# Kernel tuning notes

Measured on AMD Instinct MI355X. Metric: run time of the kernel, lower is better.

The kernel has to match this reference:

```python
import jax, jax.numpy as jnp
import numpy as np

B, S, D = 32, 2048, 1024
E, K = 64, 8
N_TAGS = 128


def setup_inputs() -> dict:
    key = jax.random.key(0)
    k1, k2, k3, k4, k5, k6 = jax.random.split(key, 6)
    hidden_states = jax.random.normal(k1, (B, S, D), dtype=jnp.float32)
    subw_indices = jax.random.randint(k2, (B, E, K), 0, S, dtype=jnp.int32)
    subw_counts = jax.random.randint(k3, (B, E), 1, K + 1, dtype=jnp.int32)
    num_entities = jax.random.randint(k4, (B,), 1, E + 1, dtype=jnp.int32)
    fc_w = jax.random.normal(k5, (N_TAGS, D), dtype=jnp.float32) * (1.0 / np.sqrt(D))
    fc_b = jax.random.normal(k6, (N_TAGS,), dtype=jnp.float32) * 0.01
    return {
        "hidden_states": hidden_states,
        "subw_indices": subw_indices,
        "subw_counts": subw_counts,
        "num_entities": num_entities,
        "fc_w": fc_w,
        "fc_b": fc_b,
    }


def reference(hidden_states, subw_indices, subw_counts, num_entities, fc_w, fc_b):
    # Gather subword embeddings: [B, E, K, D]
    flat_idx = subw_indices.reshape(B, E * K)                      # [B, E*K]
    gathered = jnp.take_along_axis(
        hidden_states, flat_idx[:, :, None], axis=1
    ).reshape(B, E, K, D)
    # Mask padded subword slots and mean-pool per entity
    subw_mask = (jnp.arange(K)[None, None, :] < subw_counts[:, :, None])  # [B,E,K]
    subw_mask = subw_mask.astype(hidden_states.dtype)
    ent_emb = jnp.einsum("bekd,bek->bed", gathered, subw_mask)
    ent_emb = ent_emb / subw_counts[:, :, None].astype(hidden_states.dtype)
    # Zero-pad entities past num_entities (original pads with zero_emb)
    ent_mask = (jnp.arange(E)[None, :] < num_entities[:, None])    # [B,E]
    ent_emb = ent_emb * ent_mask[:, :, None].astype(hidden_states.dtype)
    # fc applied to all positions (padded rows yield the bias, as in original)
    logits = jnp.einsum("bed,td->bet", ent_emb, fc_w) + fc_b
    return logits
```

## Files before the change

### kernel.cpp

```cpp
#include <hip/hip_runtime.h>

#define BB 32
#define SS 2048
#define DD 1024
#define EE 64
#define KK 8
#define TT 128
#define MM (BB * EE)

#define KSPLIT 8
#define KCHUNK (DD / KSPLIT)
#define MT 32
#define LSTR 136

typedef __attribute__((ext_vector_type(8))) short short8;
typedef __attribute__((ext_vector_type(4))) float f32x4;

__device__ __forceinline__ unsigned short f2bf(float f) {
    union { float f; unsigned int u; } v; v.f = f;
    unsigned int u = v.u + 0x7FFFu + ((v.u >> 16) & 1u);
    return (unsigned short)(u >> 16);
}

__global__ __launch_bounds__(256) void bias_init_kernel(
    const float* __restrict__ fc_b,
    float* __restrict__ out)
{
    const int i = blockIdx.x * 256 + threadIdx.x;
    float4 b = *(const float4*)(fc_b + (i & 31) * 4);
    *(float4*)(out + 4 * (size_t)i) = b;
}

__global__ __launch_bounds__(256) void fc_fused_kernel(
    const float* __restrict__ hs,
    const int*   __restrict__ subw_idx,
    const int*   __restrict__ subw_cnt,
    const int*   __restrict__ num_ent,
    const float* __restrict__ fc_w,
    float* __restrict__ out)
{
    __shared__ unsigned short As[MT][LSTR];
    __shared__ unsigned short Bs[TT][LSTR];

    const int bx = blockIdx.x;
    const int mt = bx >> 3;
    const int ks = bx & (KSPLIT - 1);
    const int t  = threadIdx.x;
    const int wid  = t >> 6;
    const int lane = t & 63;
    const int k0 = ks * KCHUNK;

    {
        const int r   = t >> 3;
        const int sub = t & 7;
        const int be  = mt * MT + r;
        const int b   = be >> 6;
        const int e   = be & 63;
        const int cnt = subw_cnt[be];
        const int ne  = num_ent[b];
        const float scale = (e < ne) ? (1.0f / (float)cnt) : 0.0f;

        const int4* ip = (const int4*)(subw_idx + (size_t)be * KK);
        const int4 i0 = ip[0];
        const int4 i1 = ip[1];
        int idx[8] = { i0.x, i0.y, i0.z, i0.w, i1.x, i1.y, i1.z, i1.w };

        const float* base = hs + (size_t)b * SS * DD + k0 + sub * 16;

        float acc[16];
        #pragma unroll
        for (int j = 0; j < 16; ++j) acc[j] = 0.f;

        #pragma unroll
        for (int half = 0; half < 2; ++half) {
            float4 v[4][4];
            #pragma unroll
            for (int k = 0; k < 4; ++k) {
                const int kk = half * 4 + k;
                const int s = (kk < cnt) ? idx[kk] : idx[0];
                const float4* p = (const float4*)(base + (size_t)s * DD);
                v[k][0] = p[0]; v[k][1] = p[1]; v[k][2] = p[2]; v[k][3] = p[3];
            }
            #pragma unroll
            for (int k = 0; k < 4; ++k) {
                const float w = ((half * 4 + k) < cnt) ? 1.0f : 0.0f;
                #pragma unroll
                for (int j = 0; j < 4; ++j) {
                    acc[4*j+0] = fmaf(w, v[k][j].x, acc[4*j+0]);
                    acc[4*j+1] = fmaf(w, v[k][j].y, acc[4*j+1]);
                    acc[4*j+2] = fmaf(w, v[k][j].z, acc[4*j+2]);
                    acc[4*j+3] = fmaf(w, v[k][j].w, acc[4*j+3]);
                }
            }
        }

        ushort4 o[4];
        #pragma unroll
        for (int j = 0; j < 4; ++j) {
            o[j].x = f2bf(acc[4*j+0] * scale);
            o[j].y = f2bf(acc[4*j+1] * scale);
            o[j].z = f2bf(acc[4*j+2] * scale);
            o[j].w = f2bf(acc[4*j+3] * scale);
        }
        *(ushort4*)&As[r][sub * 16 + 0]  = o[0];
        *(ushort4*)&As[r][sub * 16 + 4]  = o[1];
        *(ushort4*)&As[r][sub * 16 + 8]  = o[2];
        *(ushort4*)&As[r][sub * 16 + 12] = o[3];
    }

    {
        const int n = t >> 1;
        const int h = (t & 1) * 64;
        const float4* wrow = (const float4*)(fc_w + (size_t)n * DD + k0 + h);
        #pragma unroll
        for (int j = 0; j < 16; ++j) {
            float4 v = wrow[j];
            ushort4 o;
            o.x = f2bf(v.x); o.y = f2bf(v.y); o.z = f2bf(v.z); o.w = f2bf(v.w);
            *(ushort4*)&Bs[n][h + j * 4] = o;
        }
    }
    __syncthreads();

    const int msub  = (wid & 1) * 16;
    const int nbase = (wid >> 1) * 64;
    const int lm = lane & 15;
    const int lq = (lane >> 4) * 8;

    f32x4 acc0 = {0.f,0.f,0.f,0.f}, acc1 = {0.f,0.f,0.f,0.f};
    f32x4 acc2 = {0.f,0.f,0.f,0.f}, acc3 = {0.f,0.f,0.f,0.f};

    #pragma unroll
    for (int kstep = 0; kstep < KCHUNK / 32; ++kstep) {
        const int kc = kstep * 32 + lq;
        short8 a  = *(const short8*)&As[msub + lm][kc];
        short8 b0 = *(const short8*)&Bs[nbase +  0 + lm][kc];
        short8 b1 = *(const short8*)&Bs[nbase + 16 + lm][kc];
        short8 b2 = *(const short8*)&Bs[nbase + 32 + lm][kc];
        short8 b3 = *(const short8*)&Bs[nbase + 48 + lm][kc];
        acc0 = __builtin_amdgcn_mfma_f32_16x16x32_bf16(a, b0, acc0, 0, 0, 0);
        acc1 = __builtin_amdgcn_mfma_f32_16x16x32_bf16(a, b1, acc1, 0, 0, 0);
        acc2 = __builtin_amdgcn_mfma_f32_16x16x32_bf16(a, b2, acc2, 0, 0, 0);
        acc3 = __builtin_amdgcn_mfma_f32_16x16x32_bf16(a, b3, acc3, 0, 0, 0);
    }

    const int mrow = mt * MT + msub + (lane >> 4) * 4;
    const int ncol = nbase + (lane & 15);
    #pragma unroll
    for (int r = 0; r < 4; ++r) {
        const size_t base = (size_t)(mrow + r) * TT + ncol;
        atomicAdd(out + base +  0, acc0[r]);
        atomicAdd(out + base + 16, acc1[r]);
        atomicAdd(out + base + 32, acc2[r]);
        atomicAdd(out + base + 48, acc3[r]);
    }
}

extern "C" void kernel_launch(void* const* d_in, const int* in_sizes, int n_in,
                              void* d_out, int out_size, void* d_ws, size_t ws_size,
                              hipStream_t stream) {
    const float* hs       = (const float*)d_in[0];
    const int*   subw_idx = (const int*)  d_in[1];
    const int*   subw_cnt = (const int*)  d_in[2];
    const int*   num_ent  = (const int*)  d_in[3];
    const float* fc_w     = (const float*)d_in[4];
    const float* fc_b     = (const float*)d_in[5];
    float*       out      = (float*)d_out;

    bias_init_kernel<<<(MM * TT / 4) / 256, 256, 0, stream>>>(fc_b, out);
    fc_fused_kernel<<<(MM / MT) * KSPLIT, 256, 0, stream>>>(
        hs, subw_idx, subw_cnt, num_ent, fc_w, out);
}
```

Before: 319.4 us.

## Split into pooling kernel and full-K GEMM kernel via bf16 workspace

Replaces the fused split-K kernel and the bias-init kernel with two kernels. The first pools entity embeddings into a bf16 workspace, skips gather loads for padded entities, and converts fc_w to bf16 once. The second runs a full-K MFMA GEMM per 32-row tile and writes bias-added outputs directly, with no atomics. This removes the atomic adds, the repeated per-block fc_w conversion and the bias pass. In exchange it adds a workspace round trip, and the GEMM grid has only 64 blocks, which may underuse the GPU.

```diff
diff --git a/kernel.cpp b/kernel.cpp
--- a/kernel.cpp
+++ b/kernel.cpp
@@ -8,11 +8,6 @@
 #define TT 128
 #define MM (BB * EE)
 
-#define KSPLIT 8
-#define KCHUNK (DD / KSPLIT)
-#define MT 32
-#define LSTR 136
-
 typedef __attribute__((ext_vector_type(8))) short short8;
 typedef __attribute__((ext_vector_type(4))) float f32x4;
 
@@ -22,137 +17,161 @@
     return (unsigned short)(u >> 16);
 }
 
-__global__ __launch_bounds__(256) void bias_init_kernel(
-    const float* __restrict__ fc_b,
-    float* __restrict__ out)
-{
-    const int i = blockIdx.x * 256 + threadIdx.x;
-    float4 b = *(const float4*)(fc_b + (i & 31) * 4);
-    *(float4*)(out + 4 * (size_t)i) = b;
-}
+#define W_OFF ((size_t)MM * DD)
 
-__global__ __launch_bounds__(256) void fc_fused_kernel(
+__global__ __launch_bounds__(256) void pool_kernel(
     const float* __restrict__ hs,
     const int*   __restrict__ subw_idx,
     const int*   __restrict__ subw_cnt,
     const int*   __restrict__ num_ent,
     const float* __restrict__ fc_w,
-    float* __restrict__ out)
+    unsigned short* __restrict__ wsb)
 {
-    __shared__ unsigned short As[MT][LSTR];
-    __shared__ unsigned short Bs[TT][LSTR];
+    const int t = threadIdx.x;
+    if (blockIdx.x < 1024) {
+        const int wave = t >> 6;
+        const int lane = t & 63;
+        const int gid  = blockIdx.x * 4 + wave;
+        const int be   = gid >> 1;
+        const int half = gid & 1;
+        const int b = be >> 6;
+        const int e = be & 63;
+        const int ne = num_ent[b];
 
-    const int bx = blockIdx.x;
-    const int mt = bx >> 3;
-    const int ks = bx & (KSPLIT - 1);
-    const int t  = threadIdx.x;
-    const int wid  = t >> 6;
-    const int lane = t & 63;
-    const int k0 = ks * KCHUNK;
+        unsigned short* outp = wsb + (size_t)be * DD + half * 512 + lane * 8;
 
-    {
-        const int r   = t >> 3;
-        const int sub = t & 7;
-        const int be  = mt * MT + r;
-        const int b   = be >> 6;
-        const int e   = be & 63;
+        if (e >= ne) {
+            ushort4 z = {0, 0, 0, 0};
+            *(ushort4*)(outp)     = z;
+            *(ushort4*)(outp + 4) = z;
+            return;
+        }
+
         const int cnt = subw_cnt[be];
-        const int ne  = num_ent[b];
-        const float scale = (e < ne) ? (1.0f / (float)cnt) : 0.0f;
-
+        const float scale = 1.0f / (float)cnt;
         const int4* ip = (const int4*)(subw_idx + (size_t)be * KK);
         const int4 i0 = ip[0];
         const int4 i1 = ip[1];
-        int idx[8] = { i0.x, i0.y, i0.z, i0.w, i1.x, i1.y, i1.z, i1.w };
+        const int idx[8] = { i0.x, i0.y, i0.z, i0.w, i1.x, i1.y, i1.z, i1.w };
 
-        const float* base = hs + (size_t)b * SS * DD + k0 + sub * 16;
+        const float* base = hs + (size_t)b * SS * DD + half * 512 + lane * 8;
 
-        float acc[16];
+        float4 v[8][2];
         #pragma unroll
-        for (int j = 0; j < 16; ++j) acc[j] = 0.f;
-
-        #pragma unroll
-        for (int half = 0; half < 2; ++half) {
-            float4 v[4][4];
-            #pragma unroll
-            for (int k = 0; k < 4; ++k) {
-                const int kk = half * 4 + k;
-                const int s = (kk < cnt) ? idx[kk] : idx[0];
-                const float4* p = (const float4*)(base + (size_t)s * DD);
-                v[k][0] = p[0]; v[k][1] = p[1]; v[k][2] = p[2]; v[k][3] = p[3];
-            }
-            #pragma unroll
-            for (int k = 0; k < 4; ++k) {
-                const float w = ((half * 4 + k) < cnt) ? 1.0f : 0.0f;
-                #pragma unroll
-                for (int j = 0; j < 4; ++j) {
-                    acc[4*j+0] = fmaf(w, v[k][j].x, acc[4*j+0]);
-                    acc[4*j+1] = fmaf(w, v[k][j].y, acc[4*j+1]);
-                    acc[4*j+2] = fmaf(w, v[k][j].z, acc[4*j+2]);
-                    acc[4*j+3] = fmaf(w, v[k][j].w, acc[4*j+3]);
-                }
-            }
+        for (int k = 0; k < 8; ++k) {
+            const int s = (k < cnt) ? idx[k] : idx[0];
+            const float4* p = (const float4*)(base + (size_t)s * DD);
+            v[k][0] = p[0];
+            v[k][1] = p[1];
         }
 
-        ushort4 o[4];
+        float acc[8];
         #pragma unroll
-        for (int j = 0; j < 4; ++j) {
-            o[j].x = f2bf(acc[4*j+0] * scale);
-            o[j].y = f2bf(acc[4*j+1] * scale);
-            o[j].z = f2bf(acc[4*j+2] * scale);
-            o[j].w = f2bf(acc[4*j+3] * scale);
+        for (int j = 0; j < 8; ++j) acc[j] = 0.f;
+        #pragma unroll
+        for (int k = 0; k < 8; ++k) {
+            const float w = (k < cnt) ? 1.0f : 0.0f;
+            acc[0] = fmaf(w, v[k][0].x, acc[0]);
+            acc[1] = fmaf(w, v[k][0].y, acc[1]);
+            acc[2] = fmaf(w, v[k][0].z, acc[2]);
+            acc[3] = fmaf(w, v[k][0].w, acc[3]);
+            acc[4] = fmaf(w, v[k][1].x, acc[4]);
+            acc[5] = fmaf(w, v[k][1].y, acc[5]);
+            acc[6] = fmaf(w, v[k][1].z, acc[6]);
+            acc[7] = fmaf(w, v[k][1].w, acc[7]);
         }
-        *(ushort4*)&As[r][sub * 16 + 0]  = o[0];
-        *(ushort4*)&As[r][sub * 16 + 4]  = o[1];
-        *(ushort4*)&As[r][sub * 16 + 8]  = o[2];
-        *(ushort4*)&As[r][sub * 16 + 12] = o[3];
-    }
 
-    {
-        const int n = t >> 1;
-        const int h = (t & 1) * 64;
-        const float4* wrow = (const float4*)(fc_w + (size_t)n * DD + k0 + h);
+        ushort4 o0, o1;
+        o0.x = f2bf(acc[0] * scale); o0.y = f2bf(acc[1] * scale);
+        o0.z = f2bf(acc[2] * scale); o0.w = f2bf(acc[3] * scale);
+        o1.x = f2bf(acc[4] * scale); o1.y = f2bf(acc[5] * scale);
+        o1.z = f2bf(acc[6] * scale); o1.w = f2bf(acc[7] * scale);
+        *(ushort4*)(outp)     = o0;
+        *(ushort4*)(outp + 4) = o1;
+    } else {
+        const int wb  = blockIdx.x - 1024;
+        const int row = wb * 8 + (t >> 5);
+        const int col = (t & 31) * 32;
+        const float4* src = (const float4*)(fc_w + (size_t)row * DD + col);
+        unsigned short* dst = wsb + W_OFF + (size_t)row * DD + col;
         #pragma unroll
-        for (int j = 0; j < 16; ++j) {
-            float4 v = wrow[j];
+        for (int j = 0; j < 8; ++j) {
+            float4 x = src[j];
             ushort4 o;
-            o.x = f2bf(v.x); o.y = f2bf(v.y); o.z = f2bf(v.z); o.w = f2bf(v.w);
-            *(ushort4*)&Bs[n][h + j * 4] = o;
+            o.x = f2bf(x.x); o.y = f2bf(x.y); o.z = f2bf(x.z); o.w = f2bf(x.w);
+            *(ushort4*)(dst + j * 4) = o;
         }
     }
-    __syncthreads();
+}
+
+#define LSTR2 72
+
+__global__ __launch_bounds__(256) void gemm_kernel(
+    const unsigned short* __restrict__ wsb,
+    const float* __restrict__ fc_b,
+    float* __restrict__ out)
+{
+    __shared__ unsigned short As[32][LSTR2];
+    __shared__ unsigned short Ws[TT][LSTR2];
+
+    const int t    = threadIdx.x;
+    const int wid  = t >> 6;
+    const int lane = t & 63;
+    const int mbase = blockIdx.x * 32;
 
     const int msub  = (wid & 1) * 16;
     const int nbase = (wid >> 1) * 64;
     const int lm = lane & 15;
     const int lq = (lane >> 4) * 8;
 
+    const int ar = t >> 3;
+    const int ac = (t & 7) * 8;
+    const int wr = t >> 1;
+    const int wc = (t & 1) * 32;
+
     f32x4 acc0 = {0.f,0.f,0.f,0.f}, acc1 = {0.f,0.f,0.f,0.f};
     f32x4 acc2 = {0.f,0.f,0.f,0.f}, acc3 = {0.f,0.f,0.f,0.f};
 
-    #pragma unroll
-    for (int kstep = 0; kstep < KCHUNK / 32; ++kstep) {
-        const int kc = kstep * 32 + lq;
-        short8 a  = *(const short8*)&As[msub + lm][kc];
-        short8 b0 = *(const short8*)&Bs[nbase +  0 + lm][kc];
-        short8 b1 = *(const short8*)&Bs[nbase + 16 + lm][kc];
-        short8 b2 = *(const short8*)&Bs[nbase + 32 + lm][kc];
-        short8 b3 = *(const short8*)&Bs[nbase + 48 + lm][kc];
-        acc0 = __builtin_amdgcn_mfma_f32_16x16x32_bf16(a, b0, acc0, 0, 0, 0);
-        acc1 = __builtin_amdgcn_mfma_f32_16x16x32_bf16(a, b1, acc1, 0, 0, 0);
-        acc2 = __builtin_amdgcn_mfma_f32_16x16x32_bf16(a, b2, acc2, 0, 0, 0);
-        acc3 = __builtin_amdgcn_mfma_f32_16x16x32_bf16(a, b3, acc3, 0, 0, 0);
+    const unsigned short* Ag = wsb + (size_t)(mbase + ar) * DD + ac;
+    const unsigned short* Wg = wsb + W_OFF + (size_t)wr * DD + wc;
+
+    for (int kt = 0; kt < DD / 64; ++kt) {
+        const int k0 = kt * 64;
+        *(short8*)&As[ar][ac] = *(const short8*)(Ag + k0);
+        #pragma unroll
+        for (int j = 0; j < 4; ++j)
+            *(short8*)&Ws[wr][wc + 8 * j] = *(const short8*)(Wg + k0 + 8 * j);
+        __syncthreads();
+
+        #pragma unroll
+        for (int ksub = 0; ksub < 2; ++ksub) {
+            const int kc = ksub * 32 + lq;
+            short8 a  = *(const short8*)&As[msub + lm][kc];
+            short8 b0 = *(const short8*)&Ws[nbase +  0 + lm][kc];
+            short8 b1 = *(const short8*)&Ws[nbase + 16 + lm][kc];
+            short8 b2 = *(const short8*)&Ws[nbase + 32 + lm][kc];
+            short8 b3 = *(const short8*)&Ws[nbase + 48 + lm][kc];
+            acc0 = __builtin_amdgcn_mfma_f32_16x16x32_bf16(a, b0, acc0, 0, 0, 0);
+            acc1 = __builtin_amdgcn_mfma_f32_16x16x32_bf16(a, b1, acc1, 0, 0, 0);
+            acc2 = __builtin_amdgcn_mfma_f32_16x16x32_bf16(a, b2, acc2, 0, 0, 0);
+            acc3 = __builtin_amdgcn_mfma_f32_16x16x32_bf16(a, b3, acc3, 0, 0, 0);
+        }
+        __syncthreads();
     }
 
-    const int mrow = mt * MT + msub + (lane >> 4) * 4;
-    const int ncol = nbase + (lane & 15);
+    const int mrow = mbase + msub + (lane >> 4) * 4;
+    const int ncol = nbase + lm;
+    const float bb0 = fc_b[ncol +  0];
+    const float bb1 = fc_b[ncol + 16];
+    const float bb2 = fc_b[ncol + 32];
+    const float bb3 = fc_b[ncol + 48];
     #pragma unroll
     for (int r = 0; r < 4; ++r) {
         const size_t base = (size_t)(mrow + r) * TT + ncol;
-        atomicAdd(out + base +  0, acc0[r]);
-        atomicAdd(out + base + 16, acc1[r]);
-        atomicAdd(out + base + 32, acc2[r]);
-        atomicAdd(out + base + 48, acc3[r]);
+        out[base +  0] = acc0[r] + bb0;
+        out[base + 16] = acc1[r] + bb1;
+        out[base + 32] = acc2[r] + bb2;
+        out[base + 48] = acc3[r] + bb3;
     }
 }
 
@@ -166,8 +185,9 @@
     const float* fc_w     = (const float*)d_in[4];
     const float* fc_b     = (const float*)d_in[5];
     float*       out      = (float*)d_out;
+    unsigned short* wsb   = (unsigned short*)d_ws;
 
-    bias_init_kernel<<<(MM * TT / 4) / 256, 256, 0, stream>>>(fc_b, out);
-    fc_fused_kernel<<<(MM / MT) * KSPLIT, 256, 0, stream>>>(
-        hs, subw_idx, subw_cnt, num_ent, fc_w, out);
+    pool_kernel<<<1024 + 16, 256, 0, stream>>>(
+        hs, subw_idx, subw_cnt, num_ent, fc_w, wsb);
+    gemm_kernel<<<MM / 32, 256, 0, stream>>>(wsb, fc_b, out);
 }
```

Result: no change. 323.2 us (+1.2%).
